# Kernel tuning notes

Hardware: AMD Instinct MI355X
Metric: run time of the kernel (lower is better)

Reference implementation:

```python
import jax, jax.numpy as jnp
import numpy as np

N = 100000

def _gcn_norm(edge_index, n):
    # PyG GCNConv default: add self-loops, symmetric deg^-1/2 normalization
    loops = jnp.arange(n, dtype=edge_index.dtype)
    src = jnp.concatenate([edge_index[0], loops])
    dst = jnp.concatenate([edge_index[1], loops])
    deg = jax.ops.segment_sum(jnp.ones_like(dst, dtype=jnp.float32), dst, num_segments=n)
    dinv = jnp.where(deg > 0, jax.lax.rsqrt(deg), 0.0)
    norm = dinv[src] * dinv[dst]  # [E+N]
    return src, dst, norm

def _gcn_conv(h, W, b, src, dst, norm, n):
    # transform then gather-scale-scatter aggregate
    h = h @ W                                   # [N, out]
    out = jax.ops.segment_sum(norm[:, None] * h[src], dst, num_segments=n)
    return out + b

def _prelu(h, a):
    return jnp.where(h > 0, h, a * h)

def _dropout(h, u, p=0.5):
    # deterministic dropout: keep where u >= p, scale by 1/(1-p)
    return jnp.where(u >= p, h / (1.0 - p), 0.0)

def setup_inputs() -> dict:
    key = jax.random.key(0)
    ks = jax.random.split(key, 12)
    D, H1, H2, C, E = 512, 128, 16, 10, 1600000
    x = jax.random.normal(ks[0], (N, D), dtype=jnp.float32)
    edge_index = jax.random.randint(ks[1], (2, E), 0, N, dtype=jnp.int64)
    u1 = jax.random.uniform(ks[2], (N, H1), dtype=jnp.float32)
    u2 = jax.random.uniform(ks[3], (N, H2), dtype=jnp.float32)
    def glorot(k, shp):
        lim = np.sqrt(6.0 / (shp[0] + shp[1]))
        return jax.random.uniform(k, shp, dtype=jnp.float32, minval=-lim, maxval=lim)
    W1 = glorot(ks[4], (D, H1)); b1 = jnp.zeros((H1,), jnp.float32)
    W2 = glorot(ks[5], (H1, H2)); b2 = jnp.zeros((H2,), jnp.float32)
    fcW = glorot(ks[6], (H2, C)); fcb = jnp.zeros((C,), jnp.float32)
    a = jnp.float32(0.25)  # PReLU init (shared single param for both layers)
    return {"x": x, "edge_index": edge_index, "W1": W1, "b1": b1, "W2": W2,
            "b2": b2, "a": a, "fcW": fcW, "fcb": fcb, "u1": u1, "u2": u2}

def reference(x, edge_index, W1, b1, W2, b2, a, fcW, fcb, u1, u2):
    src, dst, norm = _gcn_norm(edge_index, N)
    feat1 = _dropout(_prelu(_gcn_conv(x, W1, b1, src, dst, norm, N), a), u1)
    feat2 = _dropout(_prelu(_gcn_conv(feat1, W2, b2, src, dst, norm, N), a), u2)
    logits = feat2 @ fcW + fcb
    return (feat2, logits)
```

## Files before the change

### kernel.cpp

```cpp
#include <hip/hip_runtime.h>
#include <hip/hip_bf16.h>
#include <stdint.h>

#define NN 100000
#define DIN 512
#define H1C 128
#define H2C 16
#define NCLS 10
#define NB_SCAN ((NN + 255) / 256)

typedef __attribute__((ext_vector_type(8))) short s16x8;
typedef __attribute__((ext_vector_type(4))) float f32x4;
typedef __attribute__((ext_vector_type(4))) unsigned short u16x4;
typedef __attribute__((ext_vector_type(8))) unsigned short u16x8;

static __device__ __forceinline__ unsigned short f2bf(float f) {
  __hip_bfloat16 h = __float2bfloat16(f);
  return *(unsigned short*)&h;
}
static __device__ __forceinline__ float bflo(unsigned u) {
  return __uint_as_float(u << 16);
}
static __device__ __forceinline__ float bfhi(unsigned u) {
  return __uint_as_float(u & 0xffff0000u);
}

__device__ __forceinline__ int ld_src(const int* __restrict__ ei, int f, int E, int i) {
  return f ? ei[2 * (size_t)i] : ei[i];
}
__device__ __forceinline__ int ld_dst(const int* __restrict__ ei, int f, int E, int i) {
  return f ? ei[2 * ((size_t)E + (size_t)i)] : ei[(size_t)E + (size_t)i];
}

__global__ void k_pre(const int* __restrict__ ei, int* __restrict__ flag,
                      int* __restrict__ deg,
                      const float* __restrict__ W1, unsigned short* __restrict__ Wt, int n) {
  int i = blockIdx.x * 256 + threadIdx.x;
  if (blockIdx.x == 0 && threadIdx.x < 64) {
    int v = ei[2 * threadIdx.x + 1];
    unsigned long long b = __ballot(v == 0);
    if (threadIdx.x == 0) *flag = (b == ~0ull) ? 1 : 0;
  }
  if (i < n) deg[i] = 0;
  if (i < H1C * DIN) {
    int nn = i >> 9, k = i & 511;
    Wt[i] = f2bf(W1[(size_t)k * H1C + nn]);
  }
}

__global__ void k_count(const int* __restrict__ ei, const int* __restrict__ flag,
                        int E, int* __restrict__ deg, int* __restrict__ rank) {
  int f = *flag;
  int base = blockIdx.x * 1024 + threadIdx.x;
  if (base + 768 < E) {
    int d0 = ld_dst(ei, f, E, base);
    int d1 = ld_dst(ei, f, E, base + 256);
    int d2 = ld_dst(ei, f, E, base + 512);
    int d3 = ld_dst(ei, f, E, base + 768);
    int r0 = atomicAdd(&deg[d0], 1);
    int r1 = atomicAdd(&deg[d1], 1);
    int r2 = atomicAdd(&deg[d2], 1);
    int r3 = atomicAdd(&deg[d3], 1);
    rank[base] = r0;
    rank[base + 256] = r1;
    rank[base + 512] = r2;
    rank[base + 768] = r3;
  } else {
#pragma unroll
    for (int k = 0; k < 4; k++) {
      int i = base + k * 256;
      if (i < E) rank[i] = atomicAdd(&deg[ld_dst(ei, f, E, i)], 1);
    }
  }
}

__global__ void k_scanA(const int* __restrict__ deg, int* __restrict__ incl,
                        int* __restrict__ bsum, float* __restrict__ dinv, int n) {
  __shared__ int s[256];
  int i = blockIdx.x * 256 + threadIdx.x;
  int v = (i < n) ? deg[i] : 0;
  if (i < n) dinv[i] = rsqrtf((float)(v + 1));
  s[threadIdx.x] = v;
  __syncthreads();
  for (int off = 1; off < 256; off <<= 1) {
    int t = (threadIdx.x >= off) ? s[threadIdx.x - off] : 0;
    __syncthreads();
    s[threadIdx.x] += t;
    __syncthreads();
  }
  if (i < n) incl[i] = s[threadIdx.x];
  if (threadIdx.x == 255) bsum[blockIdx.x] = s[255];
}

__global__ void k_scanBC(const int* __restrict__ deg, const int* __restrict__ bsum,
                         int* __restrict__ offs, int n, int E, int nb) {
  __shared__ int s[512];
  int tid = threadIdx.x;
  int v = (tid < nb) ? bsum[tid] : 0;
  s[tid] = v;
  __syncthreads();
  for (int off = 1; off < 512; off <<= 1) {
    int t = (tid >= off) ? s[tid - off] : 0;
    __syncthreads();
    s[tid] += t;
    __syncthreads();
  }
  int bid = blockIdx.x;
  int pb = (bid > 0) ? s[bid - 1] : 0;
  int i = bid * 256 + (tid & 255);
  if (tid < 256 && i < n) offs[i] = offs[i] - deg[i] + pb;
  if (bid == 0 && tid == 0) offs[n] = E;
}

__global__ void k_scatter(const int* __restrict__ ei, const int* __restrict__ flag, int E,
                          const int* __restrict__ offs, const int* __restrict__ rank,
                          const float* __restrict__ dinv, uint2* __restrict__ csr_sw) {
  int f = *flag;
  int base = blockIdx.x * 1024 + threadIdx.x;
  if (base + 768 < E) {
    int i0 = base, i1 = base + 256, i2 = base + 512, i3 = base + 768;
    int s0 = ld_src(ei, f, E, i0), d0 = ld_dst(ei, f, E, i0);
    int s1 = ld_src(ei, f, E, i1), d1 = ld_dst(ei, f, E, i1);
    int s2 = ld_src(ei, f, E, i2), d2 = ld_dst(ei, f, E, i2);
    int s3 = ld_src(ei, f, E, i3), d3 = ld_dst(ei, f, E, i3);
    int r0 = rank[i0], r1 = rank[i1], r2 = rank[i2], r3 = rank[i3];
    int o0 = offs[d0], o1 = offs[d1], o2 = offs[d2], o3 = offs[d3];
    float w0 = dinv[s0], w1 = dinv[s1], w2 = dinv[s2], w3 = dinv[s3];
    csr_sw[o0 + r0] = make_uint2((unsigned)s0, __float_as_uint(w0));
    csr_sw[o1 + r1] = make_uint2((unsigned)s1, __float_as_uint(w1));
    csr_sw[o2 + r2] = make_uint2((unsigned)s2, __float_as_uint(w2));
    csr_sw[o3 + r3] = make_uint2((unsigned)s3, __float_as_uint(w3));
  } else {
#pragma unroll
    for (int k = 0; k < 4; k++) {
      int i = base + k * 256;
      if (i < E) {
        int s = ld_src(ei, f, E, i), d = ld_dst(ei, f, E, i);
        int pos = offs[d] + rank[i];
        csr_sw[pos] = make_uint2((unsigned)s, __float_as_uint(dinv[s]));
      }
    }
  }
}

#define BM 64
#define BK 64
#define LDA 72
#define LDB 72

__global__ __launch_bounds__(256) void k_gemm1_mfma(const float* __restrict__ x,
                                                    const unsigned short* __restrict__ Wt,
                                                    unsigned int* __restrict__ h1u, int n) {
  __shared__ unsigned short As[BM * LDA];
  __shared__ unsigned short Bs[H1C * LDB];
  int tid = threadIdx.x;
  int wave = tid >> 6, lane = tid & 63;
  int wm = wave >> 1, wn = wave & 1;
  int bm = blockIdx.x * BM;
  int lrow = lane & 15, lk = (lane >> 4) * 8;

  f32x4 acc[2][4];
#pragma unroll
  for (int i = 0; i < 2; i++)
#pragma unroll
    for (int j = 0; j < 4; j++) acc[i][j] = (f32x4){0.f, 0.f, 0.f, 0.f};

  float4 areg[4];
  u16x8 breg[4];

  auto loadA = [&](int k0) {
#pragma unroll
    for (int p = 0; p < 4; p++) {
      int idx = p * 256 + tid;
      int r = idx >> 4, c4 = (idx & 15) * 4;
      int row = bm + r;
      areg[p] = make_float4(0.f, 0.f, 0.f, 0.f);
      if (row < n) areg[p] = *(const float4*)(x + (size_t)row * DIN + k0 + c4);
    }
  };
  auto loadB = [&](int k0) {
#pragma unroll
    for (int p = 0; p < 4; p++) {
      int idx = p * 256 + tid;
      int r = idx >> 3, c8 = (idx & 7) * 8;
      breg[p] = *(const u16x8*)&Wt[(size_t)r * DIN + k0 + c8];
    }
  };

  loadA(0);
  loadB(0);

  for (int k0 = 0; k0 < DIN; k0 += BK) {
#pragma unroll
    for (int p = 0; p < 4; p++) {
      int idx = p * 256 + tid;
      int r = idx >> 4, c4 = (idx & 15) * 4;
      u16x4 b4;
      b4.x = f2bf(areg[p].x); b4.y = f2bf(areg[p].y);
      b4.z = f2bf(areg[p].z); b4.w = f2bf(areg[p].w);
      *(u16x4*)&As[r * LDA + c4] = b4;
      int rb = idx >> 3, c8 = (idx & 7) * 8;
      int pr = (rb & 64) + (((rb & 1) + 2 * ((rb >> 5) & 1)) << 4) + ((rb >> 1) & 15);
      *(u16x8*)&Bs[pr * LDB + c8] = breg[p];
    }
    if (k0 + BK < DIN) {
      loadA(k0 + BK);
      loadB(k0 + BK);
    }
    __syncthreads();
#pragma unroll
    for (int kk = 0; kk < 2; kk++) {
      s16x8 a[2], b[4];
#pragma unroll
      for (int mi = 0; mi < 2; mi++)
        a[mi] = *(const s16x8*)&As[(wm * 32 + mi * 16 + lrow) * LDA + kk * 32 + lk];
#pragma unroll
      for (int nj = 0; nj < 4; nj++)
        b[nj] = *(const s16x8*)&Bs[(wn * 64 + nj * 16 + lrow) * LDB + kk * 32 + lk];
#pragma unroll
      for (int mi = 0; mi < 2; mi++)
#pragma unroll
        for (int nj = 0; nj < 4; nj++)
          acc[mi][nj] = __builtin_amdgcn_mfma_f32_16x16x32_bf16(a[mi], b[nj], acc[mi][nj], 0, 0, 0);
    }
    __syncthreads();
  }
#pragma unroll
  for (int mi = 0; mi < 2; mi++) {
#pragma unroll
    for (int r = 0; r < 4; r++) {
      int row = bm + wm * 32 + mi * 16 + (lane >> 4) * 4 + r;
      if (row < n) {
        unsigned p0 = ((unsigned)f2bf(acc[mi][1][r]) << 16) | (unsigned)f2bf(acc[mi][0][r]);
        unsigned p1 = ((unsigned)f2bf(acc[mi][3][r]) << 16) | (unsigned)f2bf(acc[mi][2][r]);
        h1u[(size_t)row * 64 + wn * 32 + lrow] = p0;
        h1u[(size_t)row * 64 + wn * 32 + 16 + lrow] = p1;
      }
    }
  }
}

__global__ __launch_bounds__(256) void k_agg1(const unsigned int* __restrict__ h1u,
                                              const uint2* __restrict__ csr_sw,
                                              const int* __restrict__ offs,
                                              const float* __restrict__ dinv,
                                              const float* __restrict__ b1,
                                              const float* __restrict__ aP,
                                              const float* __restrict__ u1,
                                              unsigned int* __restrict__ f1u, int n) {
  int wid = (blockIdx.x * 256 + threadIdx.x) >> 6;
  int lane = threadIdx.x & 63;
  if (wid >= n) return;
  int d = wid;
  int beg = offs[d], end = offs[d + 1];
  unsigned gs = h1u[(size_t)d * 64 + lane];
  float ax = 0.f, ay = 0.f;
  int e = beg;
  for (; e + 7 < end; e += 8) {
    uint2 r0 = csr_sw[e],     r1 = csr_sw[e + 1], r2 = csr_sw[e + 2], r3 = csr_sw[e + 3];
    uint2 r4 = csr_sw[e + 4], r5 = csr_sw[e + 5], r6 = csr_sw[e + 6], r7 = csr_sw[e + 7];
    unsigned g0 = h1u[(size_t)r0.x * 64 + lane];
    unsigned g1 = h1u[(size_t)r1.x * 64 + lane];
    unsigned g2 = h1u[(size_t)r2.x * 64 + lane];
    unsigned g3 = h1u[(size_t)r3.x * 64 + lane];
    unsigned g4 = h1u[(size_t)r4.x * 64 + lane];
    unsigned g5 = h1u[(size_t)r5.x * 64 + lane];
    unsigned g6 = h1u[(size_t)r6.x * 64 + lane];
    unsigned g7 = h1u[(size_t)r7.x * 64 + lane];
    float w0 = __uint_as_float(r0.y), w1 = __uint_as_float(r1.y);
    float w2 = __uint_as_float(r2.y), w3 = __uint_as_float(r3.y);
    float w4 = __uint_as_float(r4.y), w5 = __uint_as_float(r5.y);
    float w6 = __uint_as_float(r6.y), w7 = __uint_as_float(r7.y);
    ax += w0 * bflo(g0); ay += w0 * bfhi(g0);
    ax += w1 * bflo(g1); ay += w1 * bfhi(g1);
    ax += w2 * bflo(g2); ay += w2 * bfhi(g2);
    ax += w3 * bflo(g3); ay += w3 * bfhi(g3);
    ax += w4 * bflo(g4); ay += w4 * bfhi(g4);
    ax += w5 * bflo(g5); ay += w5 * bfhi(g5);
    ax += w6 * bflo(g6); ay += w6 * bfhi(g6);
    ax += w7 * bflo(g7); ay += w7 * bfhi(g7);
  }
  for (; e + 3 < end; e += 4) {
    uint2 r0 = csr_sw[e], r1 = csr_sw[e + 1], r2 = csr_sw[e + 2], r3 = csr_sw[e + 3];
    unsigned g0 = h1u[(size_t)r0.x * 64 + lane];
    unsigned g1 = h1u[(size_t)r1.x * 64 + lane];
    unsigned g2 = h1u[(size_t)r2.x * 64 + lane];
    unsigned g3 = h1u[(size_t)r3.x * 64 + lane];
    float w0 = __uint_as_float(r0.y), w1 = __uint_as_float(r1.y);
    float w2 = __uint_as_float(r2.y), w3 = __uint_as_float(r3.y);
    ax += w0 * bflo(g0); ay += w0 * bfhi(g0);
    ax += w1 * bflo(g1); ay += w1 * bfhi(g1);
    ax += w2 * bflo(g2); ay += w2 * bfhi(g2);
    ax += w3 * bflo(g3); ay += w3 * bfhi(g3);
  }
  for (; e < end; e++) {
    uint2 rr = csr_sw[e];
    float w = __uint_as_float(rr.y);
    unsigned g = h1u[(size_t)rr.x * 64 + lane];
    ax += w * bflo(g); ay += w * bfhi(g);
  }
  float di = dinv[d];
  ax = (ax + di * bflo(gs)) * di;
  ay = (ay + di * bfhi(gs)) * di;
  float2 bb = ((const float2*)b1)[lane];
  ax += bb.x; ay += bb.y;
  float al = *aP;
  ax = ax > 0.f ? ax : al * ax;
  ay = ay > 0.f ? ay : al * ay;
  float2 uu = ((const float2*)u1)[(size_t)d * 64 + lane];
  ax = (uu.x >= 0.5f) ? ax * 2.f : 0.f;
  ay = (uu.y >= 0.5f) ? ay * 2.f : 0.f;
  unsigned pk = ((unsigned)f2bf(ay) << 16) | (unsigned)f2bf(ax);
  f1u[(size_t)d * 64 + lane] = pk;
}

__global__ __launch_bounds__(256) void k_gemm2(const unsigned int* __restrict__ f1u,
                                               const float* __restrict__ W2,
                                               unsigned int* __restrict__ h2u, int n) {
  __shared__ float ws[H1C][H2C];
  __shared__ unsigned int fs[16][66];
  int tid = threadIdx.x;
#pragma unroll
  for (int p = 0; p < 8; p++) {
    int idx = tid + p * 256;
    ws[idx >> 4][idx & 15] = W2[idx];
  }
  int r0 = blockIdx.x * 16;
  {
    int r = tid >> 4, c4 = (tid & 15) * 4;
    int row = r0 + r;
    uint4 v = make_uint4(0, 0, 0, 0);
    if (row < n) v = *(const uint4*)(f1u + (size_t)row * 64 + c4);
    *(uint4*)&fs[r][c4] = v;
  }
  __syncthreads();
  int col = tid & 15, r = tid >> 4;
  float acc = 0.f;
#pragma unroll
  for (int k = 0; k < 64; k++) {
    unsigned u = fs[r][k];
    acc += bflo(u) * ws[2 * k][col] + bfhi(u) * ws[2 * k + 1][col];
  }
  int row = r0 + r;
  float accN = __shfl_xor(acc, 1, 64);
  if ((col & 1) == 0 && row < n) {
    unsigned pk = ((unsigned)f2bf(accN) << 16) | (unsigned)f2bf(acc);
    h2u[(size_t)row * 8 + (col >> 1)] = pk;
  }
}

__global__ __launch_bounds__(256) void k_agg2(const unsigned int* __restrict__ h2u,
                                              const uint2* __restrict__ csr_sw,
                                              const int* __restrict__ offs,
                                              const float* __restrict__ dinv,
                                              const float* __restrict__ b2,
                                              const float* __restrict__ aP,
                                              const float* __restrict__ u2,
                                              const float* __restrict__ fcW,
                                              const float* __restrict__ fcb,
                                              float* __restrict__ out_feat2,
                                              float* __restrict__ out_logits, int n) {
  int wid = (blockIdx.x * 256 + threadIdx.x) >> 6;
  int lane = threadIdx.x & 63;
  if (wid >= n) return;
  int d = wid;
  int g = lane >> 3, j = lane & 7;
  int beg = offs[d], end = offs[d + 1];
  unsigned gs = h2u[(size_t)d * 8 + j];
  float aa = 0.f, ab = 0.f;
  int e = beg + g;
  for (; e + 8 < end; e += 16) {
    uint2 r0 = csr_sw[e], r1 = csr_sw[e + 8];
    unsigned g0 = h2u[(size_t)r0.x * 8 + j];
    unsigned g1 = h2u[(size_t)r1.x * 8 + j];
    float w0 = __uint_as_float(r0.y), w1 = __uint_as_float(r1.y);
    aa += w0 * bflo(g0) + w1 * bflo(g1);
    ab += w0 * bfhi(g0) + w1 * bfhi(g1);
  }
  for (; e < end; e += 8) {
    uint2 rr = csr_sw[e];
    unsigned gg = h2u[(size_t)rr.x * 8 + j];
    float w = __uint_as_float(rr.y);
    aa += w * bflo(gg); ab += w * bfhi(gg);
  }
  aa += __shfl_xor(aa, 8, 64); aa += __shfl_xor(aa, 16, 64); aa += __shfl_xor(aa, 32, 64);
  ab += __shfl_xor(ab, 8, 64); ab += __shfl_xor(ab, 16, 64); ab += __shfl_xor(ab, 32, 64);
  float di = dinv[d];
  aa = (aa + di * bflo(gs)) * di;
  ab = (ab + di * bfhi(gs)) * di;
  aa += b2[2 * j]; ab += b2[2 * j + 1];
  float al = *aP;
  aa = aa > 0.f ? aa : al * aa;
  ab = ab > 0.f ? ab : al * ab;
  float2 uu = ((const float2*)(u2 + (size_t)d * H2C))[j];
  aa = (uu.x >= 0.5f) ? aa * 2.f : 0.f;
  ab = (uu.y >= 0.5f) ? ab * 2.f : 0.f;
  if (lane < 8) {
    float2 o; o.x = aa; o.y = ab;
    ((float2*)(out_feat2 + (size_t)d * H2C))[j] = o;
  }
  int c = lane & 15;
  int cc = (c < NCLS) ? c : 0;
  float lg = fcb[cc];
#pragma unroll
  for (int k = 0; k < 8; k++) {
    float va = __shfl(aa, k, 64);
    float vb = __shfl(ab, k, 64);
    lg += va * fcW[(2 * k) * NCLS + cc] + vb * fcW[(2 * k + 1) * NCLS + cc];
  }
  if (lane < NCLS) out_logits[(size_t)d * NCLS + c] = lg;
}

extern "C" void kernel_launch(void* const* d_in, const int* in_sizes, int n_in,
                              void* d_out, int out_size, void* d_ws, size_t ws_size,
                              hipStream_t stream) {
  const float* x   = (const float*)d_in[0];
  const int*   ei  = (const int*)d_in[1];
  const float* W1  = (const float*)d_in[2];
  const float* b1  = (const float*)d_in[3];
  const float* W2  = (const float*)d_in[4];
  const float* b2  = (const float*)d_in[5];
  const float* aP  = (const float*)d_in[6];
  const float* fcW = (const float*)d_in[7];
  const float* fcb = (const float*)d_in[8];
  const float* u1  = (const float*)d_in[9];
  const float* u2  = (const float*)d_in[10];
  const int E = in_sizes[1] / 2;

  float* out_feat2  = (float*)d_out;
  float* out_logits = (float*)d_out + (size_t)NN * H2C;

  char* w = (char*)d_ws;
  size_t off = 0;
  auto A = [&](size_t bytes) -> char* {
    char* p = w + off;
    off = (off + bytes + 255) & ~(size_t)255;
    return p;
  };
  int*   flag   = (int*)A(256);
  int*   deg    = (int*)A((size_t)NN * 4);
  int*   offs   = (int*)A((size_t)(NN + 1) * 4);
  float* dinv   = (float*)A((size_t)NN * 4);
  int*   bsum   = (int*)A(512 * 4);
  int*   rank   = (int*)A((size_t)E * 4);
  uint2* csr_sw = (uint2*)A((size_t)E * 8);
  unsigned int* h1u = (unsigned int*)A((size_t)NN * 64 * 4);
  unsigned int* f1u = (unsigned int*)A((size_t)NN * 64 * 4);
  unsigned int* h2u = (unsigned int*)A((size_t)NN * 8 * 4);
  unsigned short* Wt = (unsigned short*)A((size_t)H1C * DIN * 2);

  dim3 b256(256);
  int gE4 = (E + 1023) / 1024;
  int gN = (NN + 255) / 256;

  k_pre<<<gN, b256, 0, stream>>>(ei, flag, deg, W1, Wt, NN);
  k_count<<<gE4, b256, 0, stream>>>(ei, flag, E, deg, rank);
  k_scanA<<<NB_SCAN, b256, 0, stream>>>(deg, offs, bsum, dinv, NN);
  k_scanBC<<<NB_SCAN, 512, 0, stream>>>(deg, bsum, offs, NN, E, NB_SCAN);
  k_scatter<<<gE4, b256, 0, stream>>>(ei, flag, E, offs, rank, dinv, csr_sw);
  k_gemm1_mfma<<<(NN + BM - 1) / BM, b256, 0, stream>>>(x, Wt, h1u, NN);
  k_agg1<<<(NN + 3) / 4, b256, 0, stream>>>(h1u, csr_sw, offs, dinv, b1, aP, u1, f1u, NN);
  k_gemm2<<<(NN + 15) / 16, b256, 0, stream>>>(f1u, W2, h2u, NN);
  k_agg2<<<(NN + 3) / 4, b256, 0, stream>>>(h2u, csr_sw, offs, dinv, b2, aP, u2,
                                            fcW, fcb, out_feat2, out_logits, NN);
}
```

Before: 316.7 us.

## Fuse second-layer linear transform into first aggregation kernel via wave shuffles

```diff
diff --git a/kernel.cpp b/kernel.cpp
--- a/kernel.cpp
+++ b/kernel.cpp
@@ -240,14 +240,15 @@
   }
 }
 
-__global__ __launch_bounds__(256) void k_agg1(const unsigned int* __restrict__ h1u,
-                                              const uint2* __restrict__ csr_sw,
-                                              const int* __restrict__ offs,
-                                              const float* __restrict__ dinv,
-                                              const float* __restrict__ b1,
-                                              const float* __restrict__ aP,
-                                              const float* __restrict__ u1,
-                                              unsigned int* __restrict__ f1u, int n) {
+__global__ __launch_bounds__(256) void k_agg1g2(const unsigned int* __restrict__ h1u,
+                                                const uint2* __restrict__ csr_sw,
+                                                const int* __restrict__ offs,
+                                                const float* __restrict__ dinv,
+                                                const float* __restrict__ b1,
+                                                const float* __restrict__ aP,
+                                                const float* __restrict__ u1,
+                                                const float* __restrict__ W2,
+                                                unsigned int* __restrict__ h2u, int n) {
   int wid = (blockIdx.x * 256 + threadIdx.x) >> 6;
   int lane = threadIdx.x & 63;
   if (wid >= n) return;
@@ -310,42 +311,38 @@
   float2 uu = ((const float2*)u1)[(size_t)d * 64 + lane];
   ax = (uu.x >= 0.5f) ? ax * 2.f : 0.f;
   ay = (uu.y >= 0.5f) ? ay * 2.f : 0.f;
-  unsigned pk = ((unsigned)f2bf(ay) << 16) | (unsigned)f2bf(ax);
-  f1u[(size_t)d * 64 + lane] = pk;
-}
-
-__global__ __launch_bounds__(256) void k_gemm2(const unsigned int* __restrict__ f1u,
-                                               const float* __restrict__ W2,
-                                               unsigned int* __restrict__ h2u, int n) {
-  __shared__ float ws[H1C][H2C];
-  __shared__ unsigned int fs[16][66];
-  int tid = threadIdx.x;
-#pragma unroll
-  for (int p = 0; p < 8; p++) {
-    int idx = tid + p * 256;
-    ws[idx >> 4][idx & 15] = W2[idx];
-  }
-  int r0 = blockIdx.x * 16;
+
+  float p[16];
   {
-    int r = tid >> 4, c4 = (tid & 15) * 4;
-    int row = r0 + r;
-    uint4 v = make_uint4(0, 0, 0, 0);
-    if (row < n) v = *(const uint4*)(f1u + (size_t)row * 64 + c4);
-    *(uint4*)&fs[r][c4] = v;
-  }
-  __syncthreads();
-  int col = tid & 15, r = tid >> 4;
-  float acc = 0.f;
-#pragma unroll
-  for (int k = 0; k < 64; k++) {
-    unsigned u = fs[r][k];
-    acc += bflo(u) * ws[2 * k][col] + bfhi(u) * ws[2 * k + 1][col];
-  }
-  int row = r0 + r;
-  float accN = __shfl_xor(acc, 1, 64);
-  if ((col & 1) == 0 && row < n) {
-    unsigned pk = ((unsigned)f2bf(accN) << 16) | (unsigned)f2bf(acc);
-    h2u[(size_t)row * 8 + (col >> 1)] = pk;
+    const float4* w2a = (const float4*)(W2 + (size_t)(2 * lane) * H2C);
+    const float4* w2b = (const float4*)(W2 + (size_t)(2 * lane + 1) * H2C);
+#pragma unroll
+    for (int q = 0; q < 4; q++) {
+      float4 wa = w2a[q], wb = w2b[q];
+      p[4 * q + 0] = ax * wa.x + ay * wb.x;
+      p[4 * q + 1] = ax * wa.y + ay * wb.y;
+      p[4 * q + 2] = ax * wa.z + ay * wb.z;
+      p[4 * q + 3] = ax * wa.w + ay * wb.w;
+    }
+  }
+#pragma unroll
+  for (int lvl = 0; lvl < 4; lvl++) {
+    int m = 1 << lvl;
+    bool b = (lane & m) != 0;
+#pragma unroll
+    for (int j = 0; j < (8 >> lvl); j++) {
+      float keep = b ? p[2 * j + 1] : p[2 * j];
+      float send = b ? p[2 * j] : p[2 * j + 1];
+      p[j] = keep + __shfl_xor(send, m, 64);
+    }
+  }
+  float t = p[0];
+  t += __shfl_xor(t, 16, 64);
+  t += __shfl_xor(t, 32, 64);
+  float tn = __shfl_xor(t, 1, 64);
+  if (lane < 16 && (lane & 1) == 0) {
+    unsigned pk = ((unsigned)f2bf(tn) << 16) | (unsigned)f2bf(t);
+    h2u[(size_t)d * 8 + (lane >> 1)] = pk;
   }
 }
 
@@ -445,7 +442,6 @@
   int*   rank   = (int*)A((size_t)E * 4);
   uint2* csr_sw = (uint2*)A((size_t)E * 8);
   unsigned int* h1u = (unsigned int*)A((size_t)NN * 64 * 4);
-  unsigned int* f1u = (unsigned int*)A((size_t)NN * 64 * 4);
   unsigned int* h2u = (unsigned int*)A((size_t)NN * 8 * 4);
   unsigned short* Wt = (unsigned short*)A((size_t)H1C * DIN * 2);
 
@@ -459,8 +455,7 @@
   k_scanBC<<<NB_SCAN, 512, 0, stream>>>(deg, bsum, offs, NN, E, NB_SCAN);
   k_scatter<<<gE4, b256, 0, stream>>>(ei, flag, E, offs, rank, dinv, csr_sw);
   k_gemm1_mfma<<<(NN + BM - 1) / BM, b256, 0, stream>>>(x, Wt, h1u, NN);
-  k_agg1<<<(NN + 3) / 4, b256, 0, stream>>>(h1u, csr_sw, offs, dinv, b1, aP, u1, f1u, NN);
-  k_gemm2<<<(NN + 15) / 16, b256, 0, stream>>>(f1u, W2, h2u, NN);
+  k_agg1g2<<<(NN + 3) / 4, b256, 0, stream>>>(h1u, csr_sw, offs, dinv, b1, aP, u1, W2, h2u, NN);
   k_agg2<<<(NN + 3) / 4, b256, 0, stream>>>(h2u, csr_sw, offs, dinv, b2, aP, u2,
                                             fcW, fcb, out_feat2, out_logits, NN);
 }
```

Result: slower. 360.0 us (+13.7%).
